# Kernel tuning notes

Hardware: AMD Instinct MI355X
Metric: run time of the kernel (lower is better)

The kernel has to match this reference:

```python
import jax, jax.numpy as jnp
import numpy as np

LSTM = 256
NUM_CELLS = 5
BLOCKS = 6
TEMP = 5.0
TANH_C = 1.1


def setup_inputs() -> dict:
    key = jax.random.key(0)
    ks = jax.random.split(key, 8)
    s = 0.05  # small init so sigmoids/tanh stay in sane range
    return {
        "enc_w": jax.random.normal(ks[0], (5, LSTM), jnp.float32) * s,
        "w_ih": jax.random.normal(ks[1], (4 * LSTM, LSTM), jnp.float32) * s,
        "w_hh": jax.random.normal(ks[2], (4 * LSTM, LSTM), jnp.float32) * s,
        "b_ih": jax.random.normal(ks[3], (4 * LSTM,), jnp.float32) * s,
        "b_hh": jax.random.normal(ks[4], (4 * LSTM,), jnp.float32) * s,
        "w1": jax.random.normal(ks[5], (LSTM, LSTM), jnp.float32) * s,
        "w2": jax.random.normal(ks[6], (LSTM, LSTM), jnp.float32) * s,
        "v": jax.random.normal(ks[7], (LSTM,), jnp.float32) * s,
    }


def _lstm_cell(x, h, c, w_ih, w_hh, b_ih, b_hh):
    # torch.nn.LSTMCell gate order: i, f, g, o
    g = w_ih @ x + b_ih + w_hh @ h + b_hh  # [4*LSTM]
    i, f, gg, o = jnp.split(g, 4)
    i, f, o = jax.nn.sigmoid(i), jax.nn.sigmoid(f), jax.nn.sigmoid(o)
    c2 = f * c + i * jnp.tanh(gg)
    h2 = o * jnp.tanh(c2)
    return h2, c2


def _run_sampler(bkey, enc_w, w_ih, w_hh, b_ih, b_hh, w1, w2, v):
    zeros = jnp.zeros((LSTM,), jnp.float32)
    inputs = enc_w[0]  # encoder(0)
    anchors = []
    anchors_w1 = []
    prev_h = prev_c = zeros
    # first two layers: LSTM always fed zero state (faithful to source)
    for _ in range(2):
        prev_h, prev_c = _lstm_cell(inputs, zeros, zeros, w_ih, w_hh, b_ih, b_hh)
        anchors.append(zeros)
        anchors_w1.append(w1 @ prev_h)
    arc_seq, log_probs, entropies = [], [], []
    step = 0
    for layer_id in range(2, NUM_CELLS + 2):
        for _ in range(2):
            prev_h, prev_c = _lstm_cell(inputs, prev_h, prev_c, w_ih, w_hh, b_ih, b_hh)
            q = jnp.tanh(jnp.stack(anchors_w1[:layer_id]) + w2 @ prev_h)  # [layer_id, LSTM]
            logits = (q @ v) / TEMP  # [layer_id]
            logits = TANH_C * jnp.tanh(logits)
            skey = jax.random.fold_in(bkey, step); step += 1
            index = jax.random.categorical(skey, logits)
            lsm = jax.nn.log_softmax(logits)
            arc_seq.append(index)
            log_probs.append(-lsm[index])  # F.cross_entropy
            entropies.append(jax.lax.stop_gradient(-jnp.sum(lsm * jnp.exp(lsm))))
            inputs = jnp.stack(anchors[:layer_id])[index]
        prev_h, prev_c = _lstm_cell(inputs, prev_h, prev_c, w_ih, w_hh, b_ih, b_hh)
        anchors.append(prev_h)
        anchors_w1.append(w1 @ prev_h)
        inputs = enc_w[0]
    arc = jnp.stack(arc_seq)  # [2*NUM_CELLS] int
    return arc, sum(entropies), sum(log_probs), prev_c, prev_h


def reference(enc_w, w_ih, w_hh, b_ih, b_hh, w1, w2, v):
    key = jax.random.key(42)
    all_arc = []
    all_entropy = jnp.float32(0.0)
    all_log_prob = jnp.float32(0.0)
    c = h = None
    for b in range(BLOCKS):
        arc, ent, lp, c, h = _run_sampler(
            jax.random.fold_in(key, b), enc_w, w_ih, w_hh, b_ih, b_hh, w1, w2, v)
        all_arc.append(arc)
        all_entropy = all_entropy + ent
        all_log_prob = all_log_prob + lp
    return (jnp.stack(all_arc), all_log_prob, all_entropy, c[None, :], h[None, :])
```

## Files before the change

kernel.cpp:

```cpp
#include <hip/hip_runtime.h>
#include <stdint.h>


#define NBLK  6
#define PWG   8
#define TINYF 1.17549435e-38f

#define OFF_BAR   0u
#define OFF_READY 512u
#define OFF_DONE  544u
#define OFF_PART  576u
#define OFF_LPG   640u
#define OFF_HG    2176u
#define WS_NEED   14464u

#define READY_MAGIC 0x52454459
#define DONE_MAGIC  0x444f4e45

struct U2 { uint32_t x, y; };

__device__ __forceinline__ U2 tf2x32(uint32_t k0, uint32_t k1,
                                     uint32_t c0, uint32_t c1) {
  uint32_t ks2 = k0 ^ k1 ^ 0x1BD11BDAu;
  uint32_t x0 = c0 + k0, x1 = c1 + k1;
#define TFR(r) { x0 += x1; x1 = (x1 << (r)) | (x1 >> (32 - (r))); x1 ^= x0; }
  TFR(13) TFR(15) TFR(26) TFR(6)   x0 += k1;  x1 += ks2 + 1u;
  TFR(17) TFR(29) TFR(16) TFR(24)  x0 += ks2; x1 += k0 + 2u;
  TFR(13) TFR(15) TFR(26) TFR(6)   x0 += k0;  x1 += k1 + 3u;
  TFR(17) TFR(29) TFR(16) TFR(24)  x0 += k1;  x1 += ks2 + 4u;
  TFR(13) TFR(15) TFR(26) TFR(6)   x0 += ks2; x1 += k0 + 5u;
#undef TFR
  U2 r; r.x = x0; r.y = x1; return r;
}

__device__ __forceinline__ float sigf(float x) {
  return 1.0f / (1.0f + expf(-x));
}
__device__ __forceinline__ void gstore(float* p, float v) {
  __hip_atomic_store(p, v, __ATOMIC_RELAXED, __HIP_MEMORY_SCOPE_AGENT);
}
__device__ __forceinline__ float gload(const float* p) {
  return __hip_atomic_load(p, __ATOMIC_RELAXED, __HIP_MEMORY_SCOPE_AGENT);
}
__device__ __forceinline__ void istore(int* p, int v) {
  __hip_atomic_store(p, v, __ATOMIC_RELAXED, __HIP_MEMORY_SCOPE_AGENT);
}
__device__ __forceinline__ int iload(const int* p) {
  return __hip_atomic_load(p, __ATOMIC_RELAXED, __HIP_MEMORY_SCOPE_AGENT);
}

__global__ __launch_bounds__(1024) void ctrl_fused(
    const float* __restrict__ enc_w,
    const float* __restrict__ wih,
    const float* __restrict__ whh,
    const float* __restrict__ b_ih,
    const float* __restrict__ b_hh,
    const float* __restrict__ w1,
    const float* __restrict__ w2,
    const float* __restrict__ vvec,
    unsigned char* __restrict__ ws,
    float* __restrict__ out) {

  const int b = blockIdx.x & 7;
  const int p = blockIdx.x >> 3;
  if (b >= NBLK) return;
  const int tid = threadIdx.x;

  int*   slots = (int*)(ws + OFF_BAR) + b * 16;
  int*   ready = (int*)(ws + OFF_READY);
  int*   done  = (int*)(ws + OFF_DONE);
  float* part  = (float*)(ws + OFF_PART);
  float* lpg   = (float*)(ws + OFF_LPG) + b * 64;
  float* hg    = (float*)(ws + OFF_HG);

  if (p == 0 && tid == 0) {
    for (int i = 0; i < PWG; ++i) istore(&slots[i], 0);
    __builtin_amdgcn_s_waitcnt(0);
    istore(&ready[b], READY_MAGIC);
  }

  const int rl = tid >> 3, s = tid & 7;
  const int g = rl >> 5, el = rl & 31;
  const int row = g * 256 + p * 32 + el;
  const int k0 = s * 32;
  const int rl2 = tid >> 5, s2 = tid & 31;
  const int row2 = p * 32 + rl2;
  const int k02 = s2 * 8;
  const int t4 = s2 >> 2;

  __shared__ __align__(16) float hL[256], encL[256];
  __shared__ __align__(16) float anchL[4][256];
  __shared__ __align__(16) float partL[1024];
  __shared__ __align__(16) float rowSumL[128];
  __shared__ float vS[32], biasS[128], w2hS[32];
  __shared__ float aw1S[7][32];
  __shared__ float logitPGL[48];
  __shared__ int   selL;

  if (tid < 256) encL[tid] = enc_w[tid];
  if (tid < 32)  vS[tid] = vvec[p * 32 + tid];
  if (tid < 128) {
    int gg = tid >> 5, ee = tid & 31, r = gg * 256 + p * 32 + ee;
    biasS[tid] = b_ih[r] + b_hh[r];
  }

  float4 wihr[8], whhr[8];
  #pragma unroll
  for (int c = 0; c < 8; ++c) {
    int cc = (c + s) & 7;
    wihr[c] = *(const float4*)(wih + row * 256 + k0 + cc * 4);
    whhr[c] = *(const float4*)(whh + row * 256 + k0 + cc * 4);
  }
  float w1r[8], w2r[8];
  #pragma unroll
  for (int j = 0; j < 8; ++j) {
    int jj = (j + t4) & 7;
    w1r[j] = w1[row2 * 256 + k02 + jj];
    w2r[j] = w2[row2 * 256 + k02 + jj];
  }

  if (tid == 0) {
    while (iload(&ready[b]) != READY_MAGIC) __builtin_amdgcn_s_sleep(1);
  }
  __syncthreads();

  auto dotIH = [&](const float* x) {
    float acc = 0.0f;
    #pragma unroll
    for (int c = 0; c < 8; ++c) {
      int cc = (c + s) & 7;
      float4 xv = *(const float4*)(x + k0 + cc * 4);
      float4 w = wihr[c];
      acc += w.x * xv.x + w.y * xv.y + w.z * xv.z + w.w * xv.w;
    }
    return acc;
  };
  auto dotHH = [&]() {
    float acc = 0.0f;
    #pragma unroll
    for (int c = 0; c < 8; ++c) {
      int cc = (c + s) & 7;
      float4 xv = *(const float4*)(hL + k0 + cc * 4);
      float4 w = whhr[c];
      acc += w.x * xv.x + w.y * xv.y + w.z * xv.z + w.w * xv.w;
    }
    return acc;
  };
  auto dotW1 = [&]() {
    float acc = 0.0f;
    #pragma unroll
    for (int j = 0; j < 8; ++j) acc += w1r[j] * hL[k02 + ((j + t4) & 7)];
    return acc;
  };
  auto dotW2 = [&]() {
    float acc = 0.0f;
    #pragma unroll
    for (int j = 0; j < 8; ++j) acc += w2r[j] * hL[k02 + ((j + t4) & 7)];
    return acc;
  };

  const float encih = dotIH(encL);

  float cv = 0.0f;
  U2 bk = tf2x32(0u, 42u, 0u, (uint32_t)b);
  int phase = 0, wpar = 0, step = 0;
  float lpAcc = 0.0f, entAcc = 0.0f;

  auto barrier8 = [&]() {
    __syncthreads();
    ++phase;
    if (tid == 0) istore(&slots[p], phase);
    if (tid < PWG) {
      while (iload(&slots[tid]) < phase) __builtin_amdgcn_s_sleep(1);
    }
    __syncthreads();
  };

  auto cellUpdate = [&](float acc, bool isAnchor, int aid, bool lastCell) {
    partL[tid] = acc;
    __syncthreads();
    if (tid < 128) {
      float ssum = 0.0f;
      #pragma unroll
      for (int j = 0; j < 8; ++j) ssum += partL[tid * 8 + j];
      rowSumL[tid] = ssum + biasS[tid];
    }
    __syncthreads();
    if (tid < 32) {
      float gi = rowSumL[tid],       gf = rowSumL[32 + tid];
      float gg2 = rowSumL[64 + tid], go = rowSumL[96 + tid];
      float c2 = sigf(gf) * cv + sigf(gi) * tanhf(gg2);
      float h2 = sigf(go) * tanhf(c2);
      cv = c2;
      int e = p * 32 + tid;
      if (!lastCell) gstore(&hg[wpar * (NBLK * 256) + b * 256 + e], h2);
      if (lastCell && b == NBLK - 1) { out[62 + e] = cv; out[318 + e] = h2; }
    }
    if (!lastCell) {
      barrier8();
      if (tid < 256) {
        float hv = gload(&hg[wpar * (NBLK * 256) + b * 256 + tid]);
        hL[tid] = hv;
        if (isAnchor) anchL[aid][tid] = hv;
      }
      wpar ^= 1;
      __syncthreads();
    }
  };

  auto doAw1 = [&](int aid) {
    float a1 = dotW1();
    a1 += __shfl_down(a1, 16, 32);
    a1 += __shfl_down(a1, 8, 32);
    a1 += __shfl_down(a1, 4, 32);
    a1 += __shfl_down(a1, 2, 32);
    a1 += __shfl_down(a1, 1, 32);
    if (s2 == 0) aw1S[aid][rl2] = a1;
    __syncthreads();
  };

  auto doSample = [&](int L) -> int {
    float a2 = dotW2();
    a2 += __shfl_down(a2, 16, 32);
    a2 += __shfl_down(a2, 8, 32);
    a2 += __shfl_down(a2, 4, 32);
    a2 += __shfl_down(a2, 2, 32);
    a2 += __shfl_down(a2, 1, 32);
    if (s2 == 0) w2hS[rl2] = a2;
    __syncthreads();
    int wv = tid >> 6, lane = tid & 63;
    if (wv < L && lane < 32) {
      float t = tanhf(aw1S[wv][lane] + w2hS[lane]) * vS[lane];
      t += __shfl_down(t, 16, 32);
      t += __shfl_down(t, 8, 32);
      t += __shfl_down(t, 4, 32);
      t += __shfl_down(t, 2, 32);
      t += __shfl_down(t, 1, 32);
      if (lane == 0) gstore(&lpg[wv * 8 + p], t);
    }
    barrier8();
    if (tid < 8 * L) logitPGL[tid] = gload(&lpg[tid]);
    __syncthreads();
    if (tid < 64) {
      float lg = 0.0f, sgum = -1e30f;
      if (tid < L) {
        float ls = 0.0f;
        for (int j = 0; j < 8; ++j) ls += logitPGL[tid * 8 + j];
        lg = 1.1f * tanhf(ls * 0.2f);
        U2 sk = tf2x32(bk.x, bk.y, 0u, (uint32_t)step);
        U2 r2 = tf2x32(sk.x, sk.y, 0u, (uint32_t)tid);
        uint32_t bits = r2.x ^ r2.y;
        float u = __uint_as_float((bits >> 9) | 0x3f800000u) - 1.0f;
        u = fmaxf(TINYF, u + TINYF);
        sgum = lg - logf(-logf(u));
      }
      int bi = 0;
      float best = __shfl(sgum, 0, 64);
      for (int j = 1; j < L; ++j) {
        float sj = __shfl(sgum, j, 64);
        if (sj > best) { best = sj; bi = j; }
      }
      float mx = __shfl(lg, 0, 64);
      for (int j = 1; j < L; ++j) mx = fmaxf(mx, __shfl(lg, j, 64));
      float se = 0.0f;
      for (int j = 0; j < L; ++j) se += expf(__shfl(lg, j, 64) - mx);
      float lse = logf(se);
      float lgbi = __shfl(lg, bi, 64);
      float es = 0.0f;
      for (int j = 0; j < L; ++j) {
        float l = __shfl(lg, j, 64) - mx - lse;
        es += l * expf(l);
      }
      if (tid == 0) {
        lpAcc += -(lgbi - mx - lse);
        entAcc += -es;
        selL = bi;
        if (p == 0) out[b * 10 + step] = (float)bi;
      }
    }
    __syncthreads();
    step++;
    return selL;
  };

  cellUpdate(encih, false, 0, false);
  doAw1(0);
  if (tid < 32) aw1S[1][tid] = aw1S[0][tid];
  __syncthreads();

  for (int L = 2; L <= 6; ++L) {
    cellUpdate(encih + dotHH(), false, 0, false);
    int s1v = doSample(L);
    {
      float acc = (s1v >= 2) ? dotIH(&anchL[s1v - 2][0]) : 0.0f;
      cellUpdate(acc + dotHH(), false, 0, false);
    }
    int s2v = doSample(L);
    {
      float acc = (s2v >= 2) ? dotIH(&anchL[s2v - 2][0]) : 0.0f;
      cellUpdate(acc + dotHH(), L < 6, L - 2, L == 6);
    }
    if (L < 6) doAw1(L);
  }

  if (p == 0 && tid == 0) {
    gstore(&part[2 * b], lpAcc);
    gstore(&part[2 * b + 1], entAcc);
    __builtin_amdgcn_s_waitcnt(0);
    istore(&done[b], DONE_MAGIC);
    if (b == NBLK - 1) {
      float lp = 0.0f, en = 0.0f;
      for (int j = 0; j < NBLK; ++j) {
        while (iload(&done[j]) != DONE_MAGIC) __builtin_amdgcn_s_sleep(1);
        lp += gload(&part[2 * j]);
        en += gload(&part[2 * j + 1]);
      }
      out[60] = lp;
      out[61] = en;
    }
  }
}

extern "C" void kernel_launch(void* const* d_in, const int* in_sizes, int n_in,
                              void* d_out, int out_size, void* d_ws, size_t ws_size,
                              hipStream_t stream) {
  const float* enc = (const float*)d_in[0];
  const float* wih = (const float*)d_in[1];
  const float* whh = (const float*)d_in[2];
  const float* bih = (const float*)d_in[3];
  const float* bhh = (const float*)d_in[4];
  const float* w1  = (const float*)d_in[5];
  const float* w2  = (const float*)d_in[6];
  const float* v   = (const float*)d_in[7];
  unsigned char* ws = (unsigned char*)d_ws;
  float* out = (float*)d_out;

  ctrl_fused<<<dim3(64), dim3(1024), 0, stream>>>(
      enc, wih, whh, bih, bhh, w1, w2, v, ws, out);
}
```

Measured before the change: 170.1 us.

## Replace phase barriers with tagged h exchange and fixed-point atomic W1/W2 projections

Removes the per-step counter barrier across the 8 workgroups of each block. Each workgroup now publishes its h slice as 64-bit values tagged with the step number, and the others poll those tags directly. Each workgroup also computes partial W1/W2 projections from its own h slice and adds them into a triple-buffered global accumulator with integer atomics in fixed-point. This folds the separate W1/W2 and logit-reduction phases into the cell step and removes one cross-workgroup exchange per sample. The cost is fixed-point quantization error, many more atomics, and subtle ordering risks, since the accumulator is read after only the h-tag wait.

```diff
diff --git a/kernel.cpp b/kernel.cpp
--- a/kernel.cpp
+++ b/kernel.cpp
@@ -5,18 +5,17 @@
 #define NBLK  6
 #define PWG   8
 #define TINYF 1.17549435e-38f
-
-#define OFF_BAR   0u
-#define OFF_READY 512u
-#define OFF_DONE  544u
-#define OFF_PART  576u
-#define OFF_LPG   640u
-#define OFF_HG    2176u
-#define WS_NEED   14464u
-
+#define FXS   67108864.0f
 #define READY_MAGIC 0x52454459
 #define DONE_MAGIC  0x444f4e45
 
+#define OFF_READY 0u
+#define OFF_DONE  192u
+#define OFF_PART  224u
+#define OFF_HP    320u
+#define OFF_ACC   24896u
+
+typedef unsigned long long u64;
 struct U2 { uint32_t x, y; };
 
 __device__ __forceinline__ U2 tf2x32(uint32_t k0, uint32_t k1,
@@ -36,16 +35,22 @@
 __device__ __forceinline__ float sigf(float x) {
   return 1.0f / (1.0f + expf(-x));
 }
-__device__ __forceinline__ void gstore(float* p, float v) {
-  __hip_atomic_store(p, v, __ATOMIC_RELAXED, __HIP_MEMORY_SCOPE_AGENT);
-}
-__device__ __forceinline__ float gload(const float* p) {
-  return __hip_atomic_load(p, __ATOMIC_RELAXED, __HIP_MEMORY_SCOPE_AGENT);
-}
 __device__ __forceinline__ void istore(int* p, int v) {
   __hip_atomic_store(p, v, __ATOMIC_RELAXED, __HIP_MEMORY_SCOPE_AGENT);
 }
 __device__ __forceinline__ int iload(const int* p) {
+  return __hip_atomic_load(p, __ATOMIC_RELAXED, __HIP_MEMORY_SCOPE_AGENT);
+}
+__device__ __forceinline__ void hstore(u64* p, u64 v) {
+  __hip_atomic_store(p, v, __ATOMIC_RELAXED, __HIP_MEMORY_SCOPE_AGENT);
+}
+__device__ __forceinline__ u64 hload(const u64* p) {
+  return __hip_atomic_load(p, __ATOMIC_RELAXED, __HIP_MEMORY_SCOPE_AGENT);
+}
+__device__ __forceinline__ void fstore(float* p, float v) {
+  __hip_atomic_store(p, v, __ATOMIC_RELAXED, __HIP_MEMORY_SCOPE_AGENT);
+}
+__device__ __forceinline__ float fload(const float* p) {
   return __hip_atomic_load(p, __ATOMIC_RELAXED, __HIP_MEMORY_SCOPE_AGENT);
 }
 
@@ -66,39 +71,27 @@
   if (b >= NBLK) return;
   const int tid = threadIdx.x;
 
-  int*   slots = (int*)(ws + OFF_BAR) + b * 16;
   int*   ready = (int*)(ws + OFF_READY);
   int*   done  = (int*)(ws + OFF_DONE);
   float* part  = (float*)(ws + OFF_PART);
-  float* lpg   = (float*)(ws + OFF_LPG) + b * 64;
-  float* hg    = (float*)(ws + OFF_HG);
-
-  if (p == 0 && tid == 0) {
-    for (int i = 0; i < PWG; ++i) istore(&slots[i], 0);
-    __builtin_amdgcn_s_waitcnt(0);
-    istore(&ready[b], READY_MAGIC);
-  }
+  u64*   hp    = (u64*)(ws + OFF_HP);
+  int*   acc   = (int*)(ws + OFF_ACC);
 
   const int rl = tid >> 3, s = tid & 7;
   const int g = rl >> 5, el = rl & 31;
   const int row = g * 256 + p * 32 + el;
   const int k0 = s * 32;
-  const int rl2 = tid >> 5, s2 = tid & 31;
-  const int row2 = p * 32 + rl2;
-  const int k02 = s2 * 8;
-  const int t4 = s2 >> 2;
-
-  __shared__ __align__(16) float hL[256], encL[256];
+  const int rr = tid & 255, ks = tid >> 2 >> 6;
+
+  __shared__ __align__(16) float hL[256], encL[256], vL[256];
   __shared__ __align__(16) float anchL[4][256];
   __shared__ __align__(16) float partL[1024];
-  __shared__ __align__(16) float rowSumL[128];
-  __shared__ float vS[32], biasS[128], w2hS[32];
-  __shared__ float aw1S[7][32];
-  __shared__ float logitPGL[48];
+  __shared__ __align__(16) float w2hS[256], aw1S[6][256];
+  __shared__ float rowSumL[128], biasS[128], h2S[32];
+  __shared__ float logitL[8];
   __shared__ int   selL;
 
-  if (tid < 256) encL[tid] = enc_w[tid];
-  if (tid < 32)  vS[tid] = vvec[p * 32 + tid];
+  if (tid < 256) { encL[tid] = enc_w[tid]; vL[tid] = vvec[tid]; }
   if (tid < 128) {
     int gg = tid >> 5, ee = tid & 31, r = gg * 256 + p * 32 + ee;
     biasS[tid] = b_ih[r] + b_hh[r];
@@ -111,73 +104,54 @@
     wihr[c] = *(const float4*)(wih + row * 256 + k0 + cc * 4);
     whhr[c] = *(const float4*)(whh + row * 256 + k0 + cc * 4);
   }
-  float w1r[8], w2r[8];
+  float w1c[8], w2c[8];
   #pragma unroll
   for (int j = 0; j < 8; ++j) {
-    int jj = (j + t4) & 7;
-    w1r[j] = w1[row2 * 256 + k02 + jj];
-    w2r[j] = w2[row2 * 256 + k02 + jj];
-  }
-
-  if (tid == 0) {
-    while (iload(&ready[b]) != READY_MAGIC) __builtin_amdgcn_s_sleep(1);
-  }
+    w1c[j] = w1[rr * 256 + p * 32 + ks * 8 + j];
+    w2c[j] = w2[rr * 256 + p * 32 + ks * 8 + j];
+  }
+
+  if (tid < 32) istore(&acc[1 * (NBLK * 256) + b * 256 + p * 32 + tid], 0);
   __syncthreads();
+  if (tid == 0) istore(&ready[b * 8 + p], READY_MAGIC);
+  if (tid < 8) {
+    while (iload(&ready[b * 8 + tid]) != READY_MAGIC)
+      __builtin_amdgcn_s_sleep(1);
+  }
+  __syncthreads();
 
   auto dotIH = [&](const float* x) {
-    float acc = 0.0f;
+    float a = 0.0f;
     #pragma unroll
     for (int c = 0; c < 8; ++c) {
       int cc = (c + s) & 7;
       float4 xv = *(const float4*)(x + k0 + cc * 4);
       float4 w = wihr[c];
-      acc += w.x * xv.x + w.y * xv.y + w.z * xv.z + w.w * xv.w;
-    }
-    return acc;
+      a += w.x * xv.x + w.y * xv.y + w.z * xv.z + w.w * xv.w;
+    }
+    return a;
   };
   auto dotHH = [&]() {
-    float acc = 0.0f;
+    float a = 0.0f;
     #pragma unroll
     for (int c = 0; c < 8; ++c) {
       int cc = (c + s) & 7;
       float4 xv = *(const float4*)(hL + k0 + cc * 4);
       float4 w = whhr[c];
-      acc += w.x * xv.x + w.y * xv.y + w.z * xv.z + w.w * xv.w;
-    }
-    return acc;
-  };
-  auto dotW1 = [&]() {
-    float acc = 0.0f;
-    #pragma unroll
-    for (int j = 0; j < 8; ++j) acc += w1r[j] * hL[k02 + ((j + t4) & 7)];
-    return acc;
-  };
-  auto dotW2 = [&]() {
-    float acc = 0.0f;
-    #pragma unroll
-    for (int j = 0; j < 8; ++j) acc += w2r[j] * hL[k02 + ((j + t4) & 7)];
-    return acc;
+      a += w.x * xv.x + w.y * xv.y + w.z * xv.z + w.w * xv.w;
+    }
+    return a;
   };
 
   const float encih = dotIH(encL);
 
   float cv = 0.0f;
   U2 bk = tf2x32(0u, 42u, 0u, (uint32_t)b);
-  int phase = 0, wpar = 0, step = 0;
+  int k = 1, step = 0;
   float lpAcc = 0.0f, entAcc = 0.0f;
 
-  auto barrier8 = [&]() {
-    __syncthreads();
-    ++phase;
-    if (tid == 0) istore(&slots[p], phase);
-    if (tid < PWG) {
-      while (iload(&slots[tid]) < phase) __builtin_amdgcn_s_sleep(1);
-    }
-    __syncthreads();
-  };
-
-  auto cellUpdate = [&](float acc, bool isAnchor, int aid, bool lastCell) {
-    partL[tid] = acc;
+  auto cell = [&](float gacc, int mode, int aid, int cid) {
+    partL[tid] = gacc;
     __syncthreads();
     if (tid < 128) {
       float ssum = 0.0f;
@@ -192,61 +166,71 @@
       float c2 = sigf(gf) * cv + sigf(gi) * tanhf(gg2);
       float h2 = sigf(go) * tanhf(c2);
       cv = c2;
-      int e = p * 32 + tid;
-      if (!lastCell) gstore(&hg[wpar * (NBLK * 256) + b * 256 + e], h2);
-      if (lastCell && b == NBLK - 1) { out[62 + e] = cv; out[318 + e] = h2; }
-    }
-    if (!lastCell) {
-      barrier8();
-      if (tid < 256) {
-        float hv = gload(&hg[wpar * (NBLK * 256) + b * 256 + tid]);
-        hL[tid] = hv;
-        if (isAnchor) anchL[aid][tid] = hv;
-      }
-      wpar ^= 1;
-      __syncthreads();
-    }
+      h2S[tid] = h2;
+      if (mode == 2 && b == NBLK - 1) {
+        out[62 + p * 32 + tid] = cv;
+        out[318 + p * 32 + tid] = h2;
+      }
+    }
+    __syncthreads();
+    if (mode == 2) return;
+
+    {
+      const float* wc = (mode == 1) ? w1c : w2c;
+      float yp = 0.0f;
+      #pragma unroll
+      for (int j = 0; j < 8; ++j) yp += wc[j] * h2S[ks * 8 + j];
+      atomicAdd(&acc[(k % 3) * (NBLK * 256) + b * 256 + rr],
+                __float2int_rn(yp * FXS));
+      if (tid < 32)
+        istore(&acc[((k + 1) % 3) * (NBLK * 256) + b * 256 + p * 32 + tid], 0);
+    }
+    __syncthreads();
+    if (tid < 32) {
+      u64 pk = ((u64)(uint32_t)k << 32) | (u64)__float_as_uint(h2S[tid]);
+      hstore(&hp[(k & 1) * (NBLK * 256) + b * 256 + p * 32 + tid], pk);
+    }
+    if (tid < 256) {
+      u64 v;
+      const u64* src = &hp[(k & 1) * (NBLK * 256) + b * 256 + tid];
+      while ((int)(hload(src) >> 32) != k) __builtin_amdgcn_s_sleep(1);
+      v = hload(src);
+      float hv = __uint_as_float((uint32_t)v);
+      hL[tid] = hv;
+      if (mode == 1 && cid >= 0) anchL[cid][tid] = hv;
+    }
+    __syncthreads();
+    if (tid < 256) {
+      int iv = iload(&acc[(k % 3) * (NBLK * 256) + b * 256 + tid]);
+      float f = (float)((double)iv * (1.0 / 67108864.0));
+      if (mode == 1) aw1S[aid][tid] = f; else w2hS[tid] = f;
+    }
+    __syncthreads();
+    ++k;
   };
 
-  auto doAw1 = [&](int aid) {
-    float a1 = dotW1();
-    a1 += __shfl_down(a1, 16, 32);
-    a1 += __shfl_down(a1, 8, 32);
-    a1 += __shfl_down(a1, 4, 32);
-    a1 += __shfl_down(a1, 2, 32);
-    a1 += __shfl_down(a1, 1, 32);
-    if (s2 == 0) aw1S[aid][rl2] = a1;
-    __syncthreads();
-  };
-
-  auto doSample = [&](int L) -> int {
-    float a2 = dotW2();
-    a2 += __shfl_down(a2, 16, 32);
-    a2 += __shfl_down(a2, 8, 32);
-    a2 += __shfl_down(a2, 4, 32);
-    a2 += __shfl_down(a2, 2, 32);
-    a2 += __shfl_down(a2, 1, 32);
-    if (s2 == 0) w2hS[rl2] = a2;
-    __syncthreads();
+  auto sample = [&](int L) -> int {
     int wv = tid >> 6, lane = tid & 63;
-    if (wv < L && lane < 32) {
-      float t = tanhf(aw1S[wv][lane] + w2hS[lane]) * vS[lane];
-      t += __shfl_down(t, 16, 32);
-      t += __shfl_down(t, 8, 32);
-      t += __shfl_down(t, 4, 32);
-      t += __shfl_down(t, 2, 32);
-      t += __shfl_down(t, 1, 32);
-      if (lane == 0) gstore(&lpg[wv * 8 + p], t);
-    }
-    barrier8();
-    if (tid < 8 * L) logitPGL[tid] = gload(&lpg[tid]);
+    if (wv < L) {
+      float a = 0.0f;
+      #pragma unroll
+      for (int j = 0; j < 4; ++j) {
+        int kk = lane * 4 + j;
+        a += tanhf(aw1S[wv][kk] + w2hS[kk]) * vL[kk];
+      }
+      a += __shfl_down(a, 32);
+      a += __shfl_down(a, 16);
+      a += __shfl_down(a, 8);
+      a += __shfl_down(a, 4);
+      a += __shfl_down(a, 2);
+      a += __shfl_down(a, 1);
+      if (lane == 0) logitL[wv] = a;
+    }
     __syncthreads();
     if (tid < 64) {
       float lg = 0.0f, sgum = -1e30f;
       if (tid < L) {
-        float ls = 0.0f;
-        for (int j = 0; j < 8; ++j) ls += logitPGL[tid * 8 + j];
-        lg = 1.1f * tanhf(ls * 0.2f);
+        lg = 1.1f * tanhf(logitL[tid] * 0.2f);
         U2 sk = tf2x32(bk.x, bk.y, 0u, (uint32_t)step);
         U2 r2 = tf2x32(sk.x, sk.y, 0u, (uint32_t)tid);
         uint32_t bits = r2.x ^ r2.y;
@@ -283,37 +267,36 @@
     return selL;
   };
 
-  cellUpdate(encih, false, 0, false);
-  doAw1(0);
-  if (tid < 32) aw1S[1][tid] = aw1S[0][tid];
+  cell(encih, 1, 0, -1);
+  if (tid < 256) aw1S[1][tid] = aw1S[0][tid];
   __syncthreads();
 
   for (int L = 2; L <= 6; ++L) {
-    cellUpdate(encih + dotHH(), false, 0, false);
-    int s1v = doSample(L);
+    cell(encih + dotHH(), 0, 0, -1);
+    int s1v = sample(L);
     {
-      float acc = (s1v >= 2) ? dotIH(&anchL[s1v - 2][0]) : 0.0f;
-      cellUpdate(acc + dotHH(), false, 0, false);
-    }
-    int s2v = doSample(L);
+      float a = (s1v >= 2) ? dotIH(&anchL[s1v - 2][0]) : 0.0f;
+      cell(a + dotHH(), 0, 0, -1);
+    }
+    int s2v = sample(L);
     {
-      float acc = (s2v >= 2) ? dotIH(&anchL[s2v - 2][0]) : 0.0f;
-      cellUpdate(acc + dotHH(), L < 6, L - 2, L == 6);
-    }
-    if (L < 6) doAw1(L);
+      float a = (s2v >= 2) ? dotIH(&anchL[s2v - 2][0]) : 0.0f;
+      if (L < 6) cell(a + dotHH(), 1, L, L - 2);
+      else       cell(a + dotHH(), 2, 0, -1);
+    }
   }
 
   if (p == 0 && tid == 0) {
-    gstore(&part[2 * b], lpAcc);
-    gstore(&part[2 * b + 1], entAcc);
+    fstore(&part[2 * b], lpAcc);
+    fstore(&part[2 * b + 1], entAcc);
     __builtin_amdgcn_s_waitcnt(0);
     istore(&done[b], DONE_MAGIC);
     if (b == NBLK - 1) {
       float lp = 0.0f, en = 0.0f;
       for (int j = 0; j < NBLK; ++j) {
         while (iload(&done[j]) != DONE_MAGIC) __builtin_amdgcn_s_sleep(1);
-        lp += gload(&part[2 * j]);
-        en += gload(&part[2 * j + 1]);
+        lp += fload(&part[2 * j]);
+        en += fload(&part[2 * j + 1]);
       }
       out[60] = lp;
       out[61] = en;
```

Measured after the change: 155.7 us. 8.5% less time.
